# Kernel tuning notes

Measured on AMD Instinct MI355X. Metric: run time of the kernel, lower is better.

## Reference

```python
import jax, jax.numpy as jnp
import numpy as np

C_IN = 128
D_K = 256
D_V = 256
N_HEAD = 8
H = 192
W = 192
REGION = 3
TEMPER = int(np.sqrt(D_K))  # int(sqrt(d_k)) per the torch module


def setup_inputs() -> dict:
    key = jax.random.key(0)
    k1, k2, k3, k4 = jax.random.split(key, 4)
    scale = 1.0 / np.sqrt(C_IN).astype(np.float32)
    x = jax.random.normal(k1, (1, C_IN, H, W), dtype=jnp.float32)
    wq = jax.random.normal(k2, (D_K, C_IN), dtype=jnp.float32) * scale
    wk = jax.random.normal(k3, (D_K, C_IN), dtype=jnp.float32) * scale
    wv = jax.random.normal(k4, (D_V, C_IN), dtype=jnp.float32) * scale
    return {"x": x, "wq": wq, "wk": wk, "wv": wv}


def _stretch(t):
    # Equivalent of the fixed Conv3d 'stretch' trick: for each (i, j) in the
    # 3x3 region, channel 3*i+j holds the input shifted by (i-1, j-1), zero-padded.
    # t: [b, d, H, W] -> [b, 9, d, H, W]
    b, d, h, w = t.shape
    tp = jnp.pad(t, ((0, 0), (0, 0), (1, 1), (1, 1)))
    return jnp.stack(
        [tp[:, :, i:i + h, j:j + w] for i in range(REGION) for j in range(REGION)],
        axis=1,
    )


def reference(x, wq, wk, wv):
    b = x.shape[0]  # must be 1 (module's broadcast only works for batch 1)
    dkh = D_K // N_HEAD
    dvh = D_V // N_HEAD
    r2 = REGION * REGION
    # 1x1 conv projections == channel matmuls
    q = jnp.einsum('oc,bchw->bohw', wq, x)
    k = jnp.einsum('oc,bchw->bohw', wk, x)
    v = jnp.einsum('oc,bchw->bohw', wv, x)
    Q = _stretch(q)  # [b, 9, d_k, H, W]
    K = _stretch(k)
    V = _stretch(v)  # [b, 9, d_v, H, W]
    # elementwise QK, per-head channel sum, scale, softmax over the 9 region slots
    qk = (Q * K).reshape(b, r2, N_HEAD, dkh, H, W)
    scores = jax.nn.softmax(qk.sum(axis=3) / TEMPER, axis=1)  # [b, 9, n_head, H, W]
    # dropout is identity in eval mode (att_drop disabled for the reference)
    Vh = V.reshape(b, r2, N_HEAD, dvh, H, W)
    out = (scores[:, :, :, None] * Vh).sum(axis=1).reshape(b, D_V, H, W)
    return out
```

## Files before the change

kernel.cpp:

```cpp
#include <hip/hip_runtime.h>

#define HW_   36864
#define WI    192
#define HT    192
#define CIN   128
#define DK    256
#define NH    8
#define DKH   32

using short4_ = __attribute__((ext_vector_type(4))) short;
using short8  = __attribute__((ext_vector_type(8))) short;
using float4_ = __attribute__((ext_vector_type(4))) float;

static __device__ __forceinline__ float b2f(unsigned short u) {
    union { unsigned int i; float f; } x; x.i = ((unsigned int)u) << 16; return x.f;
}
static __device__ __forceinline__ unsigned short f2b(float f) {
    union { float f; unsigned int i; } x; x.f = f;
    unsigned int r = x.i + 0x7FFFu + ((x.i >> 16) & 1u);
    return (unsigned short)(r >> 16);
}

__global__ __launch_bounds__(256) void convw_kernel(
    const float* __restrict__ wq,
    const float* __restrict__ wk,
    const float* __restrict__ wv,
    unsigned short* __restrict__ wqkv)
{
    int id = blockIdx.x * 256 + threadIdx.x;
    int h   = id / 12288;
    int rem = id - h * 12288;
    int r   = rem >> 7;
    int c   = rem & 127;
    const float* __restrict__ s = (r < 32) ? wq : ((r < 64) ? wk : wv);
    wqkv[id] = f2b(s[(h * 32 + (r & 31)) * 128 + c]);
}

__global__ __launch_bounds__(256) void projfused2_kernel(
    const float* __restrict__ x,
    const unsigned short* __restrict__ wqkv,
    unsigned short* __restrict__ vbuf,
    float* __restrict__ sbuf)
{
    __shared__ unsigned short Sh[96 * 136];
    const int px0 = blockIdx.x * 64;
    const int t   = threadIdx.x;
    const int lane = t & 63, wave = t >> 6;
    const int col  = lane & 15, quad = lane >> 4;

    #pragma unroll 4
    for (int i = 0; i < 32; ++i) {
        int id = i * 256 + t;
        int c = id >> 6, p = id & 63;
        Sh[p * 136 + c] = f2b(x[c * HW_ + px0 + p]);
    }
    __syncthreads();

    short8 bfrag[4];
    {
        int n = wave * 16 + col;
        #pragma unroll
        for (int kt = 0; kt < 4; ++kt)
            bfrag[kt] = *(const short8*)&Sh[n * 136 + kt * 32 + quad * 8];
    }

    for (int head = 0; head < 8; ++head) {
        __syncthreads();
        const unsigned short* __restrict__ Ag = wqkv + head * 96 * 128;
        #pragma unroll
        for (int i = 0; i < 6; ++i) {
            int id = i * 256 + t;
            int row = id >> 4, c8 = id & 15;
            *(short8*)&Sh[row * 136 + c8 * 8] = *(const short8*)&Ag[row * 128 + c8 * 8];
        }
        __syncthreads();

        float4_ acc[6];
        #pragma unroll
        for (int mt = 0; mt < 6; ++mt)
            acc[mt] = (float4_){0.f, 0.f, 0.f, 0.f};

        #pragma unroll
        for (int mt = 0; mt < 6; ++mt) {
            #pragma unroll
            for (int kt = 0; kt < 4; ++kt) {
                short8 a = *(const short8*)&Sh[(mt * 16 + col) * 136 + kt * 32 + quad * 8];
                acc[mt] = __builtin_amdgcn_mfma_f32_16x16x32_bf16(a, bfrag[kt], acc[mt], 0, 0, 0);
            }
        }

        int px = px0 + wave * 16 + col;
        float s = 0.f;
        #pragma unroll
        for (int reg = 0; reg < 4; ++reg)
            s += acc[0][reg] * acc[2][reg]
               + acc[1][reg] * acc[3][reg];
        s += __shfl_xor(s, 16, 64);
        s += __shfl_xor(s, 32, 64);
        if (quad == 0) sbuf[head * HW_ + px] = s;
        unsigned short* vp = vbuf + ((size_t)head * HW_ + px) * 32;
        short4_ v0, v1;
        #pragma unroll
        for (int reg = 0; reg < 4; ++reg) {
            v0[reg] = (short)f2b(acc[4][reg]);
            v1[reg] = (short)f2b(acc[5][reg]);
        }
        *(short4_*)&vp[quad * 4]      = v0;
        *(short4_*)&vp[16 + quad * 4] = v1;
    }
}

__global__ __launch_bounds__(256) void attn_kernel(
    const unsigned short* __restrict__ vbuf,
    const float* __restrict__ sbuf,
    float* __restrict__ out)
{
    __shared__ float tr[32][65];
    const int b    = blockIdx.x;
    const int tile = b % 576;
    const int head = b / 576;
    const int t    = threadIdx.x;
    const int pxl  = t >> 2;
    const int cg   = t & 3;
    const int px   = tile * 64 + pxl;
    const int y    = px / WI;
    const int xx   = px - y * WI;

    const float* __restrict__ Sh = sbuf + head * HW_;

    float w[9];
    int   np[9];
    float m = -1e30f;
    #pragma unroll
    for (int r = 0; r < 9; ++r) {
        int dy = r / 3 - 1, dx = r % 3 - 1;
        int ny = y + dy, nx = xx + dx;
        bool inb = (ny >= 0) && (ny < HT) && (nx >= 0) && (nx < WI);
        int idx = inb ? (ny * WI + nx) : px;
        np[r] = idx;
        float val = inb ? (Sh[idx] * 0.0625f) : 0.0f;
        w[r] = val;
        m = fmaxf(m, val);
    }
    float wsum = 0.f;
    #pragma unroll
    for (int r = 0; r < 9; ++r) {
        float e = __expf(w[r] - m);
        w[r] = e;
        wsum += e;
    }
    float inv = 1.0f / wsum;
    #pragma unroll
    for (int r = 0; r < 9; ++r) {
        int dy = r / 3 - 1, dx = r % 3 - 1;
        int ny = y + dy, nx = xx + dx;
        bool inb = (ny >= 0) && (ny < HT) && (nx >= 0) && (nx < WI);
        w[r] = inb ? (w[r] * inv) : 0.0f;
    }

    const unsigned short* __restrict__ vb = vbuf + (size_t)head * HW_ * 32;
    float acc[8] = {0.f, 0.f, 0.f, 0.f, 0.f, 0.f, 0.f, 0.f};
    #pragma unroll
    for (int r = 0; r < 9; ++r) {
        short8 v8 = *(const short8*)&vb[np[r] * 32 + cg * 8];
        #pragma unroll
        for (int j = 0; j < 8; ++j)
            acc[j] = fmaf(w[r], b2f((unsigned short)v8[j]), acc[j]);
    }
    #pragma unroll
    for (int j = 0; j < 8; ++j)
        tr[cg * 8 + j][pxl] = acc[j];
    __syncthreads();

    const int ch = t >> 3, c8 = t & 7;
    const int px0 = tile * 64;
    const size_t obase = (size_t)(head * DKH + ch) * HW_ + px0 + c8 * 8;
    float4_ o0, o1;
    #pragma unroll
    for (int j = 0; j < 4; ++j) {
        o0[j] = tr[ch][c8 * 8 + j];
        o1[j] = tr[ch][c8 * 8 + 4 + j];
    }
    float* o = out + obase;
    *(float4_*)&o[0] = o0;
    *(float4_*)&o[4] = o1;
}

extern "C" void kernel_launch(void* const* d_in, const int* in_sizes, int n_in,
                              void* d_out, int out_size, void* d_ws, size_t ws_size,
                              hipStream_t stream) {
    const float* x  = (const float*)d_in[0];
    const float* wq = (const float*)d_in[1];
    const float* wk = (const float*)d_in[2];
    const float* wv = (const float*)d_in[3];

    char* ws = (char*)d_ws;
    unsigned short* wqkv = (unsigned short*)ws;
    unsigned short* vbuf = (unsigned short*)(ws + 196608);
    float*          sbuf = (float*)(ws + 19071104);

    convw_kernel<<<384, 256, 0, stream>>>(wq, wk, wv, wqkv);
    projfused2_kernel<<<576, 256, 0, stream>>>(x, wqkv, vbuf, sbuf);
    attn_kernel<<<4608, 256, 0, stream>>>(vbuf, sbuf, (float*)d_out);
}
```

Before: 119.9 us.

## Tile attention kernel into 4x16 pixel blocks with haloed V/score staging in LDS

Each attention block now covers a 4x16 2D pixel tile instead of 64 pixels along a row. It loads a 6x18 halo of V vectors and scores into shared memory once, then reads all 9 neighbours from LDS instead of global memory. This cuts redundant global and L2 traffic for the neighbour gathers. The output store is remapped to the 2D tile, giving shorter contiguous runs (16 floats per row), and the LDS reads may bank-conflict.

```diff
diff --git a/kernel.cpp b/kernel.cpp
--- a/kernel.cpp
+++ b/kernel.cpp
@@ -115,30 +115,49 @@
     const float* __restrict__ sbuf,
     float* __restrict__ out)
 {
+    __shared__ unsigned short Vh[6][18][32];
+    __shared__ float Ssc[6][18];
     __shared__ float tr[32][65];
+
     const int b    = blockIdx.x;
     const int tile = b % 576;
     const int head = b / 576;
     const int t    = threadIdx.x;
-    const int pxl  = t >> 2;
-    const int cg   = t & 3;
-    const int px   = tile * 64 + pxl;
-    const int y    = px / WI;
-    const int xx   = px - y * WI;
-
-    const float* __restrict__ Sh = sbuf + head * HW_;
+    const int ty = tile / 12, tx = tile - ty * 12;
+    const int y0 = ty * 4, x0 = tx * 16;
+
+    const unsigned short* __restrict__ vb = vbuf + (size_t)head * HW_ * 32;
+    const float* __restrict__ Sg = sbuf + head * HW_;
+
+    for (int id = t; id < 432; id += 256) {
+        int cell = id >> 2, q = id & 3;
+        int hy = cell / 18, hx = cell - hy * 18;
+        int gy = y0 - 1 + hy; gy = gy < 0 ? 0 : (gy > HT - 1 ? HT - 1 : gy);
+        int gx = x0 - 1 + hx; gx = gx < 0 ? 0 : (gx > WI - 1 ? WI - 1 : gx);
+        *(short8*)&Vh[hy][hx][q * 8] =
+            *(const short8*)&vb[((size_t)(gy * WI + gx)) * 32 + q * 8];
+    }
+    if (t < 108) {
+        int hy = t / 18, hx = t - hy * 18;
+        int gy = y0 - 1 + hy; gy = gy < 0 ? 0 : (gy > HT - 1 ? HT - 1 : gy);
+        int gx = x0 - 1 + hx; gx = gx < 0 ? 0 : (gx > WI - 1 ? WI - 1 : gx);
+        Ssc[hy][hx] = Sg[gy * WI + gx];
+    }
+    __syncthreads();
+
+    const int pxl = t >> 2;
+    const int cg  = t & 3;
+    const int ly  = pxl >> 4, lx = pxl & 15;
+    const int y   = y0 + ly, xx = x0 + lx;
 
     float w[9];
-    int   np[9];
     float m = -1e30f;
     #pragma unroll
     for (int r = 0; r < 9; ++r) {
         int dy = r / 3 - 1, dx = r % 3 - 1;
         int ny = y + dy, nx = xx + dx;
         bool inb = (ny >= 0) && (ny < HT) && (nx >= 0) && (nx < WI);
-        int idx = inb ? (ny * WI + nx) : px;
-        np[r] = idx;
-        float val = inb ? (Sh[idx] * 0.0625f) : 0.0f;
+        float val = inb ? (Ssc[ly + dy + 1][lx + dx + 1] * 0.0625f) : 0.0f;
         w[r] = val;
         m = fmaxf(m, val);
     }
@@ -158,11 +177,11 @@
         w[r] = inb ? (w[r] * inv) : 0.0f;
     }
 
-    const unsigned short* __restrict__ vb = vbuf + (size_t)head * HW_ * 32;
     float acc[8] = {0.f, 0.f, 0.f, 0.f, 0.f, 0.f, 0.f, 0.f};
     #pragma unroll
     for (int r = 0; r < 9; ++r) {
-        short8 v8 = *(const short8*)&vb[np[r] * 32 + cg * 8];
+        int dy = r / 3 - 1, dx = r % 3 - 1;
+        short8 v8 = *(const short8*)&Vh[ly + dy + 1][lx + dx + 1][cg * 8];
         #pragma unroll
         for (int j = 0; j < 8; ++j)
             acc[j] = fmaf(w[r], b2f((unsigned short)v8[j]), acc[j]);
@@ -172,16 +191,16 @@
         tr[cg * 8 + j][pxl] = acc[j];
     __syncthreads();
 
-    const int ch = t >> 3, c8 = t & 7;
-    const int px0 = tile * 64;
-    const size_t obase = (size_t)(head * DKH + ch) * HW_ + px0 + c8 * 8;
+    const int ch   = t >> 3;
+    const int ly2  = (t >> 1) & 3;
+    const int half = t & 1;
     float4_ o0, o1;
     #pragma unroll
     for (int j = 0; j < 4; ++j) {
-        o0[j] = tr[ch][c8 * 8 + j];
-        o1[j] = tr[ch][c8 * 8 + 4 + j];
-    }
-    float* o = out + obase;
+        o0[j] = tr[ch][ly2 * 16 + half * 8 + j];
+        o1[j] = tr[ch][ly2 * 16 + half * 8 + 4 + j];
+    }
+    float* o = out + (size_t)(head * DKH + ch) * HW_ + (y0 + ly2) * WI + x0 + half * 8;
     *(float4_*)&o[0] = o0;
     *(float4_*)&o[4] = o1;
 }
```

Result: no change. 118.0 us (-1.6%).

## Fuse projection and local attention into one tiled kernel with halo recompute

Applied to the files above, without the earlier changes.

Replaces the separate projection and attention kernels with one kernel. Each block loads a 6x24 spatial tile plus a one-pixel halo of x into shared memory, computes Q/K/V for four heads with MFMA, and does the 3x3 softmax and weighted V sum directly from shared memory. This removes the global round trip of the bf16 V buffer and the score buffer. In exchange, halo pixels are recomputed, the grid drops to 512 blocks, and the output stores are strided per channel rather than vectorized.

```diff
diff --git a/kernel.cpp b/kernel.cpp
--- a/kernel.cpp
+++ b/kernel.cpp
@@ -32,158 +32,163 @@
     int rem = id - h * 12288;
     int r   = rem >> 7;
     int c   = rem & 127;
-    const float* __restrict__ s = (r < 32) ? wq : ((r < 64) ? wk : wv);
-    wqkv[id] = f2b(s[(h * 32 + (r & 31)) * 128 + c]);
-}
-
-__global__ __launch_bounds__(256) void projfused2_kernel(
+    int g   = r >> 4;
+    int gm  = g % 3;
+    int rr  = ((g >= 3) ? 16 : 0) + (r & 15);
+    const float* __restrict__ s = (gm == 0) ? wq : ((gm == 1) ? wk : wv);
+    wqkv[id] = f2b(s[(h * 32 + rr) * 128 + c]);
+}
+
+__global__ __launch_bounds__(256) void fusedattn_kernel(
     const float* __restrict__ x,
     const unsigned short* __restrict__ wqkv,
-    unsigned short* __restrict__ vbuf,
-    float* __restrict__ sbuf)
+    float* __restrict__ out)
 {
-    __shared__ unsigned short Sh[96 * 136];
-    const int px0 = blockIdx.x * 64;
-    const int t   = threadIdx.x;
+    __shared__ __align__(16) unsigned short Bs[208 * 136];
+    __shared__ __align__(16) unsigned short Vt[208 * 40];
+    __shared__ float Sc[2][208];
+
+    const int blk   = blockIdx.x;
+    const int hbase = (blk & 1) * 4;
+    const int tile  = blk >> 1;
+    const int ty = tile >> 3, tx = tile & 7;
+    const int y0 = ty * 6, x0 = tx * 24;
+    const int t    = threadIdx.x;
     const int lane = t & 63, wave = t >> 6;
     const int col  = lane & 15, quad = lane >> 4;
-
-    #pragma unroll 4
-    for (int i = 0; i < 32; ++i) {
-        int id = i * 256 + t;
-        int c = id >> 6, p = id & 63;
-        Sh[p * 136 + c] = f2b(x[c * HW_ + px0 + p]);
+    const int wm   = wave >> 1, wn = wave & 1;
+    const int ntb  = wn * 6;
+
+    short8 a[3][4];
+    {
+        const unsigned short* __restrict__ Ag = wqkv + hbase * 12288;
+        #pragma unroll
+        for (int mt = 0; mt < 3; ++mt)
+            #pragma unroll
+            for (int kt = 0; kt < 4; ++kt)
+                a[mt][kt] = *(const short8*)&Ag[(wm * 48 + mt * 16 + col) * 128 + kt * 32 + quad * 8];
+    }
+
+    if (t < 208) {
+        int hy = t / 26, hx = t - hy * 26;
+        int gy = y0 - 1 + hy; gy = gy < 0 ? 0 : (gy > HT - 1 ? HT - 1 : gy);
+        int gx = x0 - 1 + hx; gx = gx < 0 ? 0 : (gx > WI - 1 ? WI - 1 : gx);
+        const float* __restrict__ xp = x + gy * WI + gx;
+        unsigned short* bp = Bs + t * 136;
+        #pragma unroll 8
+        for (int c = 0; c < 128; ++c)
+            bp[c] = f2b(xp[(size_t)c * HW_]);
     }
     __syncthreads();
 
-    short8 bfrag[4];
-    {
-        int n = wave * 16 + col;
-        #pragma unroll
-        for (int kt = 0; kt < 4; ++kt)
-            bfrag[kt] = *(const short8*)&Sh[n * 136 + kt * 32 + quad * 8];
+    for (int hh = 0; hh < 4; ++hh) {
+        const int head = hbase + hh;
+
+        float4_ acc[3][7];
+        #pragma unroll
+        for (int mt = 0; mt < 3; ++mt)
+            #pragma unroll
+            for (int j = 0; j < 7; ++j)
+                acc[mt][j] = (float4_){0.f, 0.f, 0.f, 0.f};
+
+        #pragma unroll
+        for (int j = 0; j < 7; ++j) {
+            const int p = (ntb + j) * 16 + col;
+            short8 bb[4];
+            #pragma unroll
+            for (int kt = 0; kt < 4; ++kt)
+                bb[kt] = *(const short8*)&Bs[p * 136 + kt * 32 + quad * 8];
+            #pragma unroll
+            for (int mt = 0; mt < 3; ++mt)
+                #pragma unroll
+                for (int kt = 0; kt < 4; ++kt)
+                    acc[mt][j] = __builtin_amdgcn_mfma_f32_16x16x32_bf16(a[mt][kt], bb[kt], acc[mt][j], 0, 0, 0);
+        }
+
+        if (hh < 3) {
+            const unsigned short* __restrict__ Ag = wqkv + (head + 1) * 12288;
+            #pragma unroll
+            for (int mt = 0; mt < 3; ++mt)
+                #pragma unroll
+                for (int kt = 0; kt < 4; ++kt)
+                    a[mt][kt] = *(const short8*)&Ag[(wm * 48 + mt * 16 + col) * 128 + kt * 32 + quad * 8];
+        }
+
+        #pragma unroll
+        for (int j = 0; j < 7; ++j) {
+            const int p = (ntb + j) * 16 + col;
+            float s = 0.f;
+            #pragma unroll
+            for (int reg = 0; reg < 4; ++reg)
+                s += acc[0][j][reg] * acc[1][j][reg];
+            s += __shfl_xor(s, 16, 64);
+            s += __shfl_xor(s, 32, 64);
+            if (quad == 0) Sc[wm][p] = s;
+            short4_ v0;
+            #pragma unroll
+            for (int reg = 0; reg < 4; ++reg)
+                v0[reg] = (short)f2b(acc[2][j][reg]);
+            *(short4_*)&Vt[p * 40 + wm * 16 + quad * 4] = v0;
+        }
+        __syncthreads();
+
+        for (int idx = t; idx < 288; idx += 256) {
+            const int pxl = idx >> 1;
+            const int hg  = idx & 1;
+            const int ly  = pxl / 24, lx = pxl - ly * 24;
+            const int y   = y0 + ly, xx = x0 + lx;
+
+            float w[9];
+            float m = -1e30f;
+            #pragma unroll
+            for (int r = 0; r < 9; ++r) {
+                int dy = r / 3 - 1, dx = r % 3 - 1;
+                int ny = y + dy, nx = xx + dx;
+                bool inb = (ny >= 0) && (ny < HT) && (nx >= 0) && (nx < WI);
+                int hp = (ly + 1 + dy) * 26 + lx + 1 + dx;
+                float val = inb ? ((Sc[0][hp] + Sc[1][hp]) * 0.0625f) : 0.0f;
+                w[r] = val;
+                m = fmaxf(m, val);
+            }
+            float wsum = 0.f;
+            #pragma unroll
+            for (int r = 0; r < 9; ++r) {
+                float e = __expf(w[r] - m);
+                w[r] = e;
+                wsum += e;
+            }
+            float inv = 1.0f / wsum;
+            #pragma unroll
+            for (int r = 0; r < 9; ++r) {
+                int dy = r / 3 - 1, dx = r % 3 - 1;
+                int ny = y + dy, nx = xx + dx;
+                bool inb = (ny >= 0) && (ny < HT) && (nx >= 0) && (nx < WI);
+                w[r] = inb ? (w[r] * inv) : 0.0f;
+            }
+
+            float o[16];
+            #pragma unroll
+            for (int j2 = 0; j2 < 16; ++j2) o[j2] = 0.f;
+            #pragma unroll
+            for (int r = 0; r < 9; ++r) {
+                int dy = r / 3 - 1, dx = r % 3 - 1;
+                int hp = (ly + 1 + dy) * 26 + lx + 1 + dx;
+                const unsigned short* vp = &Vt[hp * 40 + hg * 16];
+                short8 v8a = *(const short8*)&vp[0];
+                short8 v8b = *(const short8*)&vp[8];
+                #pragma unroll
+                for (int j2 = 0; j2 < 8; ++j2) {
+                    o[j2]     = fmaf(w[r], b2f((unsigned short)v8a[j2]), o[j2]);
+                    o[8 + j2] = fmaf(w[r], b2f((unsigned short)v8b[j2]), o[8 + j2]);
+                }
+            }
+            float* op = out + (size_t)(head * DKH + hg * 16) * HW_ + y * WI + xx;
+            #pragma unroll
+            for (int j2 = 0; j2 < 16; ++j2)
+                op[(size_t)j2 * HW_] = o[j2];
+        }
+        __syncthreads();
     }
-
-    for (int head = 0; head < 8; ++head) {
-        __syncthreads();
-        const unsigned short* __restrict__ Ag = wqkv + head * 96 * 128;
-        #pragma unroll
-        for (int i = 0; i < 6; ++i) {
-            int id = i * 256 + t;
-            int row = id >> 4, c8 = id & 15;
-            *(short8*)&Sh[row * 136 + c8 * 8] = *(const short8*)&Ag[row * 128 + c8 * 8];
-        }
-        __syncthreads();
-
-        float4_ acc[6];
-        #pragma unroll
-        for (int mt = 0; mt < 6; ++mt)
-            acc[mt] = (float4_){0.f, 0.f, 0.f, 0.f};
-
-        #pragma unroll
-        for (int mt = 0; mt < 6; ++mt) {
-            #pragma unroll
-            for (int kt = 0; kt < 4; ++kt) {
-                short8 a = *(const short8*)&Sh[(mt * 16 + col) * 136 + kt * 32 + quad * 8];
-                acc[mt] = __builtin_amdgcn_mfma_f32_16x16x32_bf16(a, bfrag[kt], acc[mt], 0, 0, 0);
-            }
-        }
-
-        int px = px0 + wave * 16 + col;
-        float s = 0.f;
-        #pragma unroll
-        for (int reg = 0; reg < 4; ++reg)
-            s += acc[0][reg] * acc[2][reg]
-               + acc[1][reg] * acc[3][reg];
-        s += __shfl_xor(s, 16, 64);
-        s += __shfl_xor(s, 32, 64);
-        if (quad == 0) sbuf[head * HW_ + px] = s;
-        unsigned short* vp = vbuf + ((size_t)head * HW_ + px) * 32;
-        short4_ v0, v1;
-        #pragma unroll
-        for (int reg = 0; reg < 4; ++reg) {
-            v0[reg] = (short)f2b(acc[4][reg]);
-            v1[reg] = (short)f2b(acc[5][reg]);
-        }
-        *(short4_*)&vp[quad * 4]      = v0;
-        *(short4_*)&vp[16 + quad * 4] = v1;
-    }
-}
-
-__global__ __launch_bounds__(256) void attn_kernel(
-    const unsigned short* __restrict__ vbuf,
-    const float* __restrict__ sbuf,
-    float* __restrict__ out)
-{
-    __shared__ float tr[32][65];
-    const int b    = blockIdx.x;
-    const int tile = b % 576;
-    const int head = b / 576;
-    const int t    = threadIdx.x;
-    const int pxl  = t >> 2;
-    const int cg   = t & 3;
-    const int px   = tile * 64 + pxl;
-    const int y    = px / WI;
-    const int xx   = px - y * WI;
-
-    const float* __restrict__ Sh = sbuf + head * HW_;
-
-    float w[9];
-    int   np[9];
-    float m = -1e30f;
-    #pragma unroll
-    for (int r = 0; r < 9; ++r) {
-        int dy = r / 3 - 1, dx = r % 3 - 1;
-        int ny = y + dy, nx = xx + dx;
-        bool inb = (ny >= 0) && (ny < HT) && (nx >= 0) && (nx < WI);
-        int idx = inb ? (ny * WI + nx) : px;
-        np[r] = idx;
-        float val = inb ? (Sh[idx] * 0.0625f) : 0.0f;
-        w[r] = val;
-        m = fmaxf(m, val);
-    }
-    float wsum = 0.f;
-    #pragma unroll
-    for (int r = 0; r < 9; ++r) {
-        float e = __expf(w[r] - m);
-        w[r] = e;
-        wsum += e;
-    }
-    float inv = 1.0f / wsum;
-    #pragma unroll
-    for (int r = 0; r < 9; ++r) {
-        int dy = r / 3 - 1, dx = r % 3 - 1;
-        int ny = y + dy, nx = xx + dx;
-        bool inb = (ny >= 0) && (ny < HT) && (nx >= 0) && (nx < WI);
-        w[r] = inb ? (w[r] * inv) : 0.0f;
-    }
-
-    const unsigned short* __restrict__ vb = vbuf + (size_t)head * HW_ * 32;
-    float acc[8] = {0.f, 0.f, 0.f, 0.f, 0.f, 0.f, 0.f, 0.f};
-    #pragma unroll
-    for (int r = 0; r < 9; ++r) {
-        short8 v8 = *(const short8*)&vb[np[r] * 32 + cg * 8];
-        #pragma unroll
-        for (int j = 0; j < 8; ++j)
-            acc[j] = fmaf(w[r], b2f((unsigned short)v8[j]), acc[j]);
-    }
-    #pragma unroll
-    for (int j = 0; j < 8; ++j)
-        tr[cg * 8 + j][pxl] = acc[j];
-    __syncthreads();
-
-    const int ch = t >> 3, c8 = t & 7;
-    const int px0 = tile * 64;
-    const size_t obase = (size_t)(head * DKH + ch) * HW_ + px0 + c8 * 8;
-    float4_ o0, o1;
-    #pragma unroll
-    for (int j = 0; j < 4; ++j) {
-        o0[j] = tr[ch][c8 * 8 + j];
-        o1[j] = tr[ch][c8 * 8 + 4 + j];
-    }
-    float* o = out + obase;
-    *(float4_*)&o[0] = o0;
-    *(float4_*)&o[4] = o1;
 }
 
 extern "C" void kernel_launch(void* const* d_in, const int* in_sizes, int n_in,
@@ -194,12 +199,8 @@
     const float* wk = (const float*)d_in[2];
     const float* wv = (const float*)d_in[3];
 
-    char* ws = (char*)d_ws;
-    unsigned short* wqkv = (unsigned short*)ws;
-    unsigned short* vbuf = (unsigned short*)(ws + 196608);
-    float*          sbuf = (float*)(ws + 19071104);
+    unsigned short* wqkv = (unsigned short*)d_ws;
 
     convw_kernel<<<384, 256, 0, stream>>>(wq, wk, wv, wqkv);
-    projfused2_kernel<<<576, 256, 0, stream>>>(x, wqkv, vbuf, sbuf);
-    attn_kernel<<<4608, 256, 0, stream>>>(vbuf, sbuf, (float*)d_out);
-}
+    fusedattn_kernel<<<512, 256, 0, stream>>>(x, wqkv, (float*)d_out);
+}
```

Result: faster. 117.1 us (-2.3%).
